# Optimization experiments

Hardware: AMD Instinct MI355X
Metric: run time of the kernel (lower is better)

Reference implementation:

```python
import jax, jax.numpy as jnp
import numpy as np

NUM = 8          # group_heads
ALPHA = 1000.0   # Pos_Enc alpha
BETA = 100.0     # Pos_Enc beta


def setup_inputs() -> dict:
    key = jax.random.key(0)
    ks = jax.random.split(key, 19)
    N, C, H = 16384, 64, 1024
    gs1 = H // NUM
    s = 0.02
    r = lambda k, shp: jax.random.normal(k, shp, dtype=jnp.float32) * s
    return {
        "features": jax.random.normal(ks[0], (N, C), dtype=jnp.float32),
        "fc1_w": r(ks[1], (C, H)), "fc1_b": r(ks[2], (H,)),
        "fc2_w": r(ks[3], (H, C)), "fc2_b": r(ks[4], (C,)),
        "g1_w": r(ks[5], (H, H)), "g1_b": r(ks[6], (H,)),
        "g2_w": r(ks[7], (H, H)), "g2_b": r(ks[8], (H,)),
        "gg1_w": r(ks[9], (gs1, gs1)), "gg1_b": r(ks[10], (gs1,)),
        "gg2_w": r(ks[11], (gs1, gs1)), "gg2_b": r(ks[12], (gs1,)),
        "wq": r(ks[13], (H, H)), "wk": r(ks[14], (H, H)), "wv": r(ks[15], (H, H)),
        "wq2": r(ks[16], (gs1, gs1)), "wk2": r(ks[17], (gs1, gs1)),
        "lpe": jax.random.normal(ks[18], (1,), dtype=jnp.float32) * 0.1,
    }


def _mlp(x, w1, b1, w2, b2):
    return jax.nn.relu(x @ w1 + b1) @ w2 + b2


def reference(features, fc1_w, fc1_b, fc2_w, fc2_b, g1_w, g1_b, g2_w, g2_b,
              gg1_w, gg1_b, gg2_w, gg2_b, wq, wk, wv, wq2, wk2, lpe):
    N, C = features.shape
    H = fc1_w.shape[1]
    gs1 = H // NUM   # feature-group size
    gs2 = N // NUM   # token-group size

    x = features @ fc1_w + fc1_b                      # (N, H)

    # --- attn1: per-feature-group vector attention (shared weights -> vectorized)
    xg = x.reshape(N, NUM, gs1)                       # contiguous feature slices
    q1 = xg @ wq2
    k1 = xg @ wk2
    h1 = _mlp(q1 - k1, gg1_w, gg1_b, gg2_w, gg2_b)
    attn1 = jax.nn.softmax(h1 / np.sqrt(gs1).astype(np.float32), axis=0)
    attn1 = attn1.reshape(N, H)                       # concat over groups = reshape

    # --- attn2: source bug: loop uses stale i=NUM-1, so the LAST token group
    # is processed NUM times and tiled along tokens.
    gf2 = x[(NUM - 1) * gs2:, :]                      # (gs2, H)
    q2 = gf2 @ wq
    k2 = gf2 @ wk
    h2 = _mlp(q2 - k2, g1_w, g1_b, g2_w, g2_b)
    a2 = jax.nn.softmax(h2 / np.sqrt(H).astype(np.float32), axis=0)
    attn2 = jnp.tile(a2, (NUM, 1))                    # (N, H)

    attn = attn1 + attn2
    v = x @ wv                                        # (N, H)

    # --- sinusoidal positional encoding (Pos_Enc), only coord-0 slice survives
    xyz = features[:, :3]                             # (N, 3)
    feat_dim = H // 2
    feat_range = jnp.arange(feat_dim, dtype=jnp.float32)
    dim_embed = jnp.power(jnp.float32(ALPHA), feat_range / feat_dim)
    div = BETA * xyz[..., None] / dim_embed           # (N, 3, feat_dim)
    emb = jnp.concatenate([jnp.sin(div), jnp.cos(div)], axis=-1)  # (N, 3, H)
    pe = (emb + lpe[0]) * lpe[0]
    pe0 = pe[:, 0, :]                                 # (N, H) first coordinate

    res = attn * (v + pe0)                            # elementwise einsum bmf,bmf->bmf
    out = res @ fc2_w + fc2_b + features              # residual
    return out
```

## Files before the change

kernel.cpp:

```cpp
#include <hip/hip_runtime.h>
#include <hip/hip_bf16.h>
#include <math.h>
#include <type_traits>


typedef __attribute__((ext_vector_type(8))) short short8;
typedef __attribute__((ext_vector_type(4))) float f32x4;
typedef __attribute__((ext_vector_type(4))) float float4v;

#define GLOAD_LDS16(gptr, lptr)                                                 \
    __builtin_amdgcn_global_load_lds(                                           \
        (const __attribute__((address_space(1))) void*)(gptr),                  \
        (__attribute__((address_space(3))) void*)(lptr), 16, 0, 0)

static __device__ __forceinline__ unsigned short f2bf_bits(float v) {
    __hip_bfloat16 h = __float2bfloat16(v);
    return __builtin_bit_cast(unsigned short, h);
}
static __device__ __forceinline__ float bf_bits2f(unsigned short u) {
    return __bfloat162float(__builtin_bit_cast(__hip_bfloat16, u));
}
static __device__ __forceinline__ int swz16(int r, int c16) {
    return (r << 4) + (c16 ^ (r & 7));
}
static __device__ __forceinline__ int swz_elem(int r, int c) {
    return (r << 7) + ((((c << 1) ^ ((r & 7) << 4))) >> 1);
}
static __device__ __forceinline__ int xcd_swz(int bid, int nwg) {
    return (bid & 7) * (nwg >> 3) + (bid >> 3);
}

static __device__ void conv_t_dev(const float* __restrict__ A, const float* __restrict__ Bsub,
                                  __hip_bfloat16* __restrict__ Ot, int K, int N,
                                  int bx, int by, int tid, float* t )
{
    const int n0 = bx * 32, k0 = by * 32;
    const int tx = tid & 31, ty = tid >> 5;
    #pragma unroll
    for (int j = 0; j < 4; ++j) {
        int k = k0 + ty + j * 8;
        float v = A[(long)k * N + n0 + tx];
        if (Bsub) v -= Bsub[(long)k * N + n0 + tx];
        t[(ty + j * 8) * 33 + tx] = v;
    }
    __syncthreads();
    #pragma unroll
    for (int j = 0; j < 4; ++j) {
        int n = n0 + ty + j * 8;
        Ot[(long)n * K + k0 + tx] = __float2bfloat16(t[tx * 33 + ty + j * 8]);
    }
}

static __device__ void xgemm_dev(const float* __restrict__ features,
                                 const float* __restrict__ fc1_w,
                                 const float* __restrict__ fc1_b,
                                 __hip_bfloat16* __restrict__ xb,
                                 int tile, int tid, char* smem)
{
    unsigned short* As = (unsigned short*)smem;
    unsigned short* Bs = (unsigned short*)(smem + 16384);
    const int bm = (tile >> 3) << 7, bn = (tile & 7) << 7;
    const int wid = tid >> 6, lane = tid & 63;
    const int wm = (wid >> 1) << 6, wn = (wid & 1) << 6;
    const int l15 = lane & 15, kg = lane >> 4;

    #pragma unroll
    for (int i = 0; i < 8; ++i) {
        int idx = i * 256 + tid;
        int r = idx >> 4, c4 = idx & 15;
        float4v f = *(const float4v*)(features + (long)(bm + r) * 64 + c4 * 4);
        unsigned int p0 = f2bf_bits(f[0]) | ((unsigned int)f2bf_bits(f[1]) << 16);
        unsigned int p1 = f2bf_bits(f[2]) | ((unsigned int)f2bf_bits(f[3]) << 16);
        int dst = r * 64 + (((c4 >> 1) ^ (r & 7)) << 3) + (c4 & 1) * 4;
        unsigned int* p = (unsigned int*)&As[dst];
        p[0] = p0; p[1] = p1;
    }
    #pragma unroll
    for (int i = 0; i < 8; ++i) {
        int idx = i * 256 + tid;
        int k = idx >> 5, c4b = idx & 31;
        float4v g = *(const float4v*)(fc1_w + (long)k * 1024 + bn + c4b * 4);
        #pragma unroll
        for (int q = 0; q < 4; ++q) {
            int n = c4b * 4 + q;
            Bs[n * 64 + (((k >> 3) ^ (n & 7)) << 3) + (k & 7)] = f2bf_bits(g[q]);
        }
    }
    __syncthreads();

    f32x4 acc[4][4] = {};
    #pragma unroll
    for (int ks2 = 0; ks2 < 2; ++ks2) {
        const int kslot = ks2 * 4 + kg;
        short8 af[4], bf_[4];
        #pragma unroll
        for (int m = 0; m < 4; ++m) {
            int r = wm + m * 16 + l15;
            af[m] = *(const short8*)&As[r * 64 + ((kslot ^ (r & 7)) << 3)];
        }
        #pragma unroll
        for (int n = 0; n < 4; ++n) {
            int r = wn + n * 16 + l15;
            bf_[n] = *(const short8*)&Bs[r * 64 + ((kslot ^ (r & 7)) << 3)];
        }
        #pragma unroll
        for (int m = 0; m < 4; ++m)
            #pragma unroll
            for (int n = 0; n < 4; ++n)
                acc[m][n] = __builtin_amdgcn_mfma_f32_16x16x32_bf16(
                    af[m], bf_[n], acc[m][n], 0, 0, 0);
    }
    const int rq = kg << 2;
    #pragma unroll
    for (int n = 0; n < 4; ++n) {
        const int col = bn + wn + n * 16 + l15;
        const float bv = fc1_b[col];
        #pragma unroll
        for (int m = 0; m < 4; ++m)
            #pragma unroll
            for (int j = 0; j < 4; ++j)
                xb[(long)(bm + wm + m * 16 + rq + j) * 1024 + col] =
                    __float2bfloat16(acc[m][n][j] + bv);
    }
}

__global__ __launch_bounds__(256) void prep_x_k(
    const float* __restrict__ features, const float* __restrict__ fc1_w,
    const float* __restrict__ fc1_b, const float* __restrict__ fc2_w,
    const float* __restrict__ fc2_b, const float* __restrict__ g1_w,
    const float* __restrict__ g2_w, const float* __restrict__ wq,
    const float* __restrict__ wk, const float* __restrict__ wv,
    const float* __restrict__ wq2, const float* __restrict__ wk2,
    const float* __restrict__ gg1_w, const float* __restrict__ gg2_w,
    __hip_bfloat16* __restrict__ fc2T, __hip_bfloat16* __restrict__ wdT,
    __hip_bfloat16* __restrict__ wvT, __hip_bfloat16* __restrict__ g1T,
    __hip_bfloat16* __restrict__ g2T, __hip_bfloat16* __restrict__ wd2T,
    __hip_bfloat16* __restrict__ gg1T, __hip_bfloat16* __restrict__ gg2T,
    __hip_bfloat16* __restrict__ xb, float* __restrict__ invde,
    float* __restrict__ out)
{
    __shared__ __align__(16) char smem[32768];
    float* t = (float*)smem;
    const int bid = blockIdx.x;
    const int tid = threadIdx.x;

    if (bid == 0) {
        #pragma unroll
        for (int i = 0; i < 2; ++i) {
            int idx = tid + i * 256;
            invde[idx] = exp2f(-9.96578428466209f * (float)idx * (1.f / 512.f));
        }
    } else if (bid < 257) {
        const float4v* f4 = (const float4v*)features;
        float4v* o4 = (float4v*)out;
        const float4v* b4 = (const float4v*)fc2_b;
        long base = (long)(bid - 1) * 1024;
        #pragma unroll
        for (int i = 0; i < 4; ++i) {
            long idx = base + tid + i * 256;
            o4[idx] = f4[idx] + b4[idx & 15];
        }
    } else if (bid < 1281) {
        int tt = bid - 257;  conv_t_dev(wq, wk, wdT, 1024, 1024, tt & 31, tt >> 5, tid, t);
    } else if (bid < 2305) {
        int tt = bid - 1281; conv_t_dev(wv, nullptr, wvT, 1024, 1024, tt & 31, tt >> 5, tid, t);
    } else if (bid < 3329) {
        int tt = bid - 2305; conv_t_dev(g1_w, nullptr, g1T, 1024, 1024, tt & 31, tt >> 5, tid, t);
    } else if (bid < 4353) {
        int tt = bid - 3329; conv_t_dev(g2_w, nullptr, g2T, 1024, 1024, tt & 31, tt >> 5, tid, t);
    } else if (bid < 4417) {
        int tt = bid - 4353; conv_t_dev(fc2_w, nullptr, fc2T, 1024, 64, tt & 1, tt >> 1, tid, t);
    } else if (bid < 4433) {
        int tt = bid - 4417; conv_t_dev(wq2, wk2, wd2T, 128, 128, tt & 3, tt >> 2, tid, t);
    } else if (bid < 4449) {
        int tt = bid - 4433; conv_t_dev(gg1_w, nullptr, gg1T, 128, 128, tt & 3, tt >> 2, tid, t);
    } else if (bid < 4465) {
        int tt = bid - 4449; conv_t_dev(gg2_w, nullptr, gg2T, 128, 128, tt & 3, tt >> 2, tid, t);
    } else {
        xgemm_dev(features, fc1_w, fc1_b, xb, bid - 4465, tid, smem);
    }
}

template <int OP, bool CS>
static __device__ void gemm6464_dev(
    const __hip_bfloat16* __restrict__ A, const __hip_bfloat16* __restrict__ Bt,
    const float* __restrict__ bias, __hip_bfloat16* __restrict__ Co,
    float scale, float* __restrict__ pcs, int swz, int tid, char* smem)
{
    const int wid = tid >> 6, lane = tid & 63;
    const int bm = (swz >> 4) << 6, bn = (swz & 15) << 6;
    const int wm = (wid >> 1) << 5, wn = (wid & 1) << 5;
    f32x4 acc[2][2] = {};
    const int l15 = lane & 15, kg = lane >> 4;
    const int rS = tid >> 2;
    const int c4s = (tid & 3) ^ ((rS >> 1) & 3);

#define G66_STAGE(b, k0)                                                        \
    { char* base = smem + (b) * 8192;                                           \
      GLOAD_LDS16(A + (long)(bm + rS) * 1024 + (k0) + c4s * 8,                  \
                  base + (wid << 6) * 16);                                      \
      GLOAD_LDS16(Bt + (long)(bn + rS) * 1024 + (k0) + c4s * 8,                 \
                  base + 4096 + (wid << 6) * 16); }

    G66_STAGE(0, 0);
    #pragma unroll 2
    for (int kt = 0; kt < 32; ++kt) {
        if (kt < 31) {
            G66_STAGE((kt + 1) & 1, (kt + 1) * 32);
            asm volatile("s_waitcnt vmcnt(2)" ::: "memory");
        } else {
            asm volatile("s_waitcnt vmcnt(0)" ::: "memory");
        }
        __builtin_amdgcn_s_barrier();
        __builtin_amdgcn_sched_barrier(0);
        const char* AsB = smem + (kt & 1) * 8192;
        const char* BsB = AsB + 4096;
        short8 af[2], bf_[2];
        #pragma unroll
        for (int m = 0; m < 2; ++m) {
            const int R = wm + m * 16 + l15;
            af[m] = *(const short8*)(AsB + R * 64 + ((kg ^ ((R >> 1) & 3)) << 4));
        }
        #pragma unroll
        for (int n = 0; n < 2; ++n) {
            const int R = wn + n * 16 + l15;
            bf_[n] = *(const short8*)(BsB + R * 64 + ((kg ^ ((R >> 1) & 3)) << 4));
        }
        __builtin_amdgcn_s_setprio(1);
        #pragma unroll
        for (int m = 0; m < 2; ++m)
            #pragma unroll
            for (int n = 0; n < 2; ++n)
                acc[m][n] = __builtin_amdgcn_mfma_f32_16x16x32_bf16(
                    af[m], bf_[n], acc[m][n], 0, 0, 0);
        __builtin_amdgcn_s_setprio(0);
        __builtin_amdgcn_s_barrier();
    }
#undef G66_STAGE

    const int rq = kg << 2;
    float csum[2];
    #pragma unroll
    for (int n = 0; n < 2; ++n) {
        const int col = bn + wn + n * 16 + l15;
        const float bv = bias ? bias[col] : 0.f;
        csum[n] = 0.f;
        #pragma unroll
        for (int m = 0; m < 2; ++m) {
            #pragma unroll
            for (int j = 0; j < 4; ++j) {
                const int row = bm + wm + m * 16 + rq + j;
                float cv = acc[m][n][j] + bv;
                if (OP == 1) cv = fmaxf(cv, 0.f);
                if (OP == 2) cv = __expf(cv * scale);
                if (CS) csum[n] += cv;
                Co[(long)row * 1024 + col] = __float2bfloat16(cv);
            }
        }
    }
    if (CS) {
        __syncthreads();
        float* ps = (float*)smem;
        const int slot = ((wid >> 1) << 2) | kg;
        #pragma unroll
        for (int n = 0; n < 2; ++n)
            ps[(wn + n * 16 + l15) * 8 + slot] = csum[n];
        __syncthreads();
        if (tid < 64) {
            float s = 0.f;
            #pragma unroll
            for (int q = 0; q < 8; ++q) s += ps[tid * 8 + q];
            pcs[(long)(swz >> 4) * 1024 + bn + tid] = s;
        }
    }
}

template <int OP, bool CS>
__global__ __launch_bounds__(256) void gemm6464_k(
    const __hip_bfloat16* __restrict__ A, const __hip_bfloat16* __restrict__ Bt,
    const float* __restrict__ bias, __hip_bfloat16* __restrict__ Co,
    float scale, float* __restrict__ pcs)
{
    __shared__ __align__(16) char smem[16384];
    const int swz = xcd_swz(blockIdx.y * gridDim.x + blockIdx.x, gridDim.x * gridDim.y);
    gemm6464_dev<OP, CS>(A, Bt, bias, Co, scale, pcs, swz, threadIdx.x, smem);
}

static __device__ void chain_dev(
    const __hip_bfloat16* __restrict__ xb,
    const __hip_bfloat16* __restrict__ w1T,
    const __hip_bfloat16* __restrict__ w2T,
    const __hip_bfloat16* __restrict__ w3T,
    const float* __restrict__ b2, const float* __restrict__ b3,
    __hip_bfloat16* __restrict__ e1, float* __restrict__ pcs1,
    int tileIdx, int tid, char* smem)
{
    unsigned short* act = (unsigned short*)smem;
    unsigned short* Wb  = (unsigned short*)(smem + 32768);
    const int wid = tid >> 6, lane = tid & 63;
    const int wm = (wid >> 1) << 6, wn = (wid & 1) << 6;
    const long tile = (long)tileIdx * (128 * 128);

    #pragma unroll
    for (int i = 0; i < 8; ++i) {
        int L = i * 256 + wid * 64 + lane;
        int r = L >> 4, c16o = (L & 15) ^ (r & 7);
        GLOAD_LDS16(xb + tile + r * 128 + c16o * 8,
                    (char*)act + (i * 256 + wid * 64) * 16);
        GLOAD_LDS16(w1T + r * 128 + c16o * 8,
                    (char*)Wb + (i * 256 + wid * 64) * 16);
    }
    __syncthreads();

    f32x4 acc[4][4];
    const int rq = (lane >> 4) << 2;

#define CHAIN_ZERO()                                                            \
    _Pragma("unroll") for (int m = 0; m < 4; ++m)                               \
        _Pragma("unroll") for (int n = 0; n < 4; ++n)                           \
            acc[m][n] = (f32x4){0.f, 0.f, 0.f, 0.f};

#define CHAIN_MM()                                                              \
    _Pragma("unroll") for (int ks = 0; ks < 4; ++ks) {                          \
        short8 af[4], bfv[4];                                                   \
        const int kc = ks * 4 + (lane >> 4);                                    \
        _Pragma("unroll") for (int m = 0; m < 4; ++m) {                         \
            int r = wm + m * 16 + (lane & 15);                                  \
            af[m] = *(const short8*)((const char*)act + swz16(r, kc) * 16);     \
        }                                                                       \
        _Pragma("unroll") for (int n = 0; n < 4; ++n) {                         \
            int r = wn + n * 16 + (lane & 15);                                  \
            bfv[n] = *(const short8*)((const char*)Wb + swz16(r, kc) * 16);     \
        }                                                                       \
        _Pragma("unroll") for (int m = 0; m < 4; ++m)                           \
            _Pragma("unroll") for (int n = 0; n < 4; ++n)                       \
                acc[m][n] = __builtin_amdgcn_mfma_f32_16x16x32_bf16(            \
                    af[m], bfv[n], acc[m][n], 0, 0, 0);                         \
    }

#define STAGE_W(wptr)                                                           \
    _Pragma("unroll") for (int i = 0; i < 8; ++i) {                             \
        int L = i * 256 + wid * 64 + lane;                                      \
        int r = L >> 4, c16o = (L & 15) ^ (r & 7);                              \
        GLOAD_LDS16((wptr) + r * 128 + c16o * 8,                                \
                    (char*)Wb + (i * 256 + wid * 64) * 16);                     \
    }

    CHAIN_ZERO(); CHAIN_MM();
    __syncthreads();
    STAGE_W(w2T);
    #pragma unroll
    for (int m = 0; m < 4; ++m)
        #pragma unroll
        for (int n = 0; n < 4; ++n)
            #pragma unroll
            for (int j = 0; j < 4; ++j) {
                int row = wm + m * 16 + rq + j, col = wn + n * 16 + (lane & 15);
                act[swz_elem(row, col)] = f2bf_bits(acc[m][n][j]);
            }
    __syncthreads();

    CHAIN_ZERO(); CHAIN_MM();
    __syncthreads();
    STAGE_W(w3T);
    {
        float bv[4];
        #pragma unroll
        for (int n = 0; n < 4; ++n) bv[n] = b2[wn + n * 16 + (lane & 15)];
        #pragma unroll
        for (int m = 0; m < 4; ++m)
            #pragma unroll
            for (int n = 0; n < 4; ++n)
                #pragma unroll
                for (int j = 0; j < 4; ++j) {
                    int row = wm + m * 16 + rq + j, col = wn + n * 16 + (lane & 15);
                    act[swz_elem(row, col)] = f2bf_bits(fmaxf(acc[m][n][j] + bv[n], 0.f));
                }
    }
    __syncthreads();

    CHAIN_ZERO(); CHAIN_MM();
    __syncthreads();
    {
        float bv[4];
        #pragma unroll
        for (int n = 0; n < 4; ++n) bv[n] = b3[wn + n * 16 + (lane & 15)];
        #pragma unroll
        for (int m = 0; m < 4; ++m)
            #pragma unroll
            for (int n = 0; n < 4; ++n)
                #pragma unroll
                for (int j = 0; j < 4; ++j) {
                    int row = wm + m * 16 + rq + j, col = wn + n * 16 + (lane & 15);
                    float ev = __expf((acc[m][n][j] + bv[n]) * 0.08838834764831845f);
                    act[swz_elem(row, col)] = f2bf_bits(ev);
                }
    }
    __syncthreads();

    #pragma unroll
    for (int i = 0; i < 8; ++i) {
        int idx = i * 256 + tid;
        int r = idx >> 4, c16o = idx & 15;
        short8 vd = *(const short8*)((const char*)act + swz16(r, c16o) * 16);
        *(short8*)((__hip_bfloat16*)e1 + tile + r * 128 + c16o * 8) = vd;
    }
    #pragma unroll
    for (int i = 0; i < 4; ++i) {
        int p = i * 256 + tid;
        int g = p >> 7, c = p & 127;
        float s = 0.f;
        #pragma unroll
        for (int t16 = 0; t16 < 16; ++t16) {
            int r = t16 * 8 + g;
            s += bf_bits2f(act[swz_elem(r, c)]);
        }
        pcs1[(long)tileIdx * 1024 + p] = s;
    }
#undef CHAIN_ZERO
#undef CHAIN_MM
#undef STAGE_W
}

__global__ __launch_bounds__(256) void mid_k(
    const __hip_bfloat16* __restrict__ xb, const __hip_bfloat16* __restrict__ wdT,
    __hip_bfloat16* __restrict__ d2b,
    const __hip_bfloat16* __restrict__ wd2T, const __hip_bfloat16* __restrict__ gg1T,
    const __hip_bfloat16* __restrict__ gg2T, const float* __restrict__ gg1_b,
    const float* __restrict__ gg2_b, __hip_bfloat16* __restrict__ e1,
    float* __restrict__ pcs1)
{
    __shared__ __align__(16) char smem[65536];
    const int bid = blockIdx.x, tid = threadIdx.x;
    if (bid < 512) {
        gemm6464_dev<0, false>(xb + (size_t)14336 * 1024, wdT, nullptr, d2b,
                               0.f, nullptr, xcd_swz(bid, 512), tid, smem);
    } else {
        chain_dev(xb, wd2T, gg1T, gg2T, gg1_b, gg2_b, e1, pcs1, bid - 512, tid, smem);
    }
}

__global__ __launch_bounds__(1024) void reduce_k(
    const float* __restrict__ pcs1, const float* __restrict__ pcs2,
    float* __restrict__ rcs1, float* __restrict__ rcs2)
{
    __shared__ float red[16][64];
    const int tx = threadIdx.x, ty = threadIdx.y;
    if (blockIdx.x < 16) {
        const int col = blockIdx.x * 64 + tx;
        float s = 0.f;
        for (int p = ty; p < 1024; p += 16) s += pcs1[(long)p * 1024 + col];
        red[ty][tx] = s;
        __syncthreads();
        if (ty == 0) {
            float t = 0.f;
            #pragma unroll
            for (int q = 0; q < 16; ++q) t += red[q][tx];
            rcs1[col] = 1.f / t;
        }
    } else {
        const int col = (blockIdx.x - 16) * 64 + tx;
        float s = 0.f;
        for (int p = ty; p < 32; p += 16) s += pcs2[(long)p * 1024 + col];
        red[ty][tx] = s;
        __syncthreads();
        if (ty == 0) {
            float t = 0.f;
            #pragma unroll
            for (int q = 0; q < 16; ++q) t += red[q][tx];
            rcs2[col] = 1.f / t;
        }
    }
}

__global__ __launch_bounds__(256) void gemm_v_res_out(
    const __hip_bfloat16* __restrict__ A, const __hip_bfloat16* __restrict__ Bt,
    const __hip_bfloat16* __restrict__ e1, const __hip_bfloat16* __restrict__ e2,
    const float* __restrict__ rcs1, const float* __restrict__ rcs2,
    const float* __restrict__ invde, const float* __restrict__ feats,
    const float* __restrict__ lpe, const __hip_bfloat16* __restrict__ fc2T,
    float* __restrict__ out)
{
    __shared__ __align__(16) char smem[34816];
    unsigned short* st = (unsigned short*)smem;

    const int tid = threadIdx.x;
    const int wid = tid >> 6;
    const int lane = tid & 63;
    const int swz = xcd_swz(blockIdx.y * gridDim.x + blockIdx.x, gridDim.x * gridDim.y);
    const int bm = (swz >> 3) << 7, bn = (swz & 7) << 7;
    const int wm = (wid >> 1) << 6, wn = (wid & 1) << 6;

    f32x4 acc[4][4] = {};
    const int l15 = lane & 15;
    const int kg = lane >> 4;
    const int arow = wm + l15;
    const int brow = wn + l15;

#define VR_STAGE(b, k0)                                                         \
    { char* base = smem + (b) * 16384;                                          \
      _Pragma("unroll") for (int i = 0; i < 2; ++i) {                           \
        const int idx = i * 256 + tid;                                          \
        const int r = idx >> 2;                                                 \
        const int c4s = (idx & 3) ^ ((r >> 1) & 3);                             \
        GLOAD_LDS16(A + (long)(bm + r) * 1024 + (k0) + c4s * 8,                 \
                    base + (i * 256 + wid * 64) * 16);                          \
        GLOAD_LDS16(Bt + (long)(bn + r) * 1024 + (k0) + c4s * 8,                \
                    base + 8192 + (i * 256 + wid * 64) * 16); } }

    VR_STAGE(0, 0);
    #pragma unroll 2
    for (int kt = 0; kt < 32; ++kt) {
        if (kt < 31) {
            VR_STAGE((kt + 1) & 1, (kt + 1) * 32);
            asm volatile("s_waitcnt vmcnt(4)" ::: "memory");
        } else {
            asm volatile("s_waitcnt vmcnt(0)" ::: "memory");
        }
        __builtin_amdgcn_s_barrier();
        __builtin_amdgcn_sched_barrier(0);
        const char* AsB = smem + (kt & 1) * 16384;
        const char* BsB = AsB + 8192;
        short8 af[4], bf_[4];
        #pragma unroll
        for (int m = 0; m < 4; ++m) {
            const int R = arow + m * 16;
            af[m] = *(const short8*)(AsB + R * 64 + ((kg ^ ((R >> 1) & 3)) << 4));
        }
        #pragma unroll
        for (int n = 0; n < 4; ++n) {
            const int R = brow + n * 16;
            bf_[n] = *(const short8*)(BsB + R * 64 + ((kg ^ ((R >> 1) & 3)) << 4));
        }
        __builtin_amdgcn_s_setprio(1);
        #pragma unroll
        for (int m = 0; m < 4; ++m)
            #pragma unroll
            for (int n = 0; n < 4; ++n)
                acc[m][n] = __builtin_amdgcn_mfma_f32_16x16x32_bf16(
                    af[m], bf_[n], acc[m][n], 0, 0, 0);
        __builtin_amdgcn_s_setprio(0);
        __builtin_amdgcn_s_barrier();
    }
#undef VR_STAGE

    const int rq = kg << 2;
    #pragma unroll
    for (int m = 0; m < 4; ++m)
        #pragma unroll
        for (int n = 0; n < 4; ++n)
            #pragma unroll
            for (int j = 0; j < 4; ++j)
                st[(wm + m * 16 + rq + j) * 136 + wn + n * 16 + l15] =
                    f2bf_bits(acc[m][n][j]);
    __syncthreads();

    const float lp = lpe[0];
    #pragma unroll
    for (int p = 0; p < 4; ++p) {
        const int r = p * 32 + (tid >> 3);
        const int cc = (tid & 7) << 4;
        const int grow = bm + r;
        const float angs = 100.f * feats[(long)grow * 64];
        const long goff = (long)grow * 1024 + bn + cc;
        const long goff2 = (long)(grow & 2047) * 1024 + bn + cc;
        short8 ev1[2], ev2[2], sv[2];
        ev1[0] = *(const short8*)((const unsigned short*)e1 + goff);
        ev1[1] = *(const short8*)((const unsigned short*)e1 + goff + 8);
        ev2[0] = *(const short8*)((const unsigned short*)e2 + goff2);
        ev2[1] = *(const short8*)((const unsigned short*)e2 + goff2 + 8);
        sv[0] = *(const short8*)&st[r * 136 + cc];
        sv[1] = *(const short8*)&st[r * 136 + cc + 8];
        unsigned short ov[16];
        #pragma unroll
        for (int q = 0; q < 16; ++q) {
            const int h = bn + cc + q;
            const float ang = angs * invde[h & 511];
            const float tr = (h < 512) ? __sinf(ang) : __cosf(ang);
            const float a = bf_bits2f((unsigned short)ev1[q >> 3][q & 7]) * rcs1[h] +
                            bf_bits2f((unsigned short)ev2[q >> 3][q & 7]) * rcs2[h];
            const float vv = bf_bits2f((unsigned short)sv[q >> 3][q & 7]);
            ov[q] = f2bf_bits(a * (vv + (tr + lp) * lp));
        }
        *(short8*)&st[r * 136 + cc] = *(short8*)&ov[0];
        *(short8*)&st[r * 136 + cc + 8] = *(short8*)&ov[8];
    }
    __syncthreads();

    {
        const int wmO = wid << 5;
        f32x4 aco[2][4] = {};
        #pragma unroll
        for (int ks = 0; ks < 4; ++ks) {
            short8 afo[2], bfo[4];
            #pragma unroll
            for (int m = 0; m < 2; ++m)
                afo[m] = *(const short8*)&st[(wmO + m * 16 + l15) * 136 + ks * 32 + kg * 8];
            #pragma unroll
            for (int n = 0; n < 4; ++n)
                bfo[n] = *(const short8*)((const unsigned short*)fc2T +
                                          (long)(n * 16 + l15) * 1024 + bn + ks * 32 + kg * 8);
            #pragma unroll
            for (int m = 0; m < 2; ++m)
                #pragma unroll
                for (int n = 0; n < 4; ++n)
                    aco[m][n] = __builtin_amdgcn_mfma_f32_16x16x32_bf16(
                        afo[m], bfo[n], aco[m][n], 0, 0, 0);
        }
        #pragma unroll
        for (int m = 0; m < 2; ++m)
            #pragma unroll
            for (int n = 0; n < 4; ++n)
                #pragma unroll
                for (int j = 0; j < 4; ++j) {
                    const int row = bm + wmO + m * 16 + rq + j;
                    atomicAdd(&out[(long)row * 64 + n * 16 + l15], aco[m][n][j]);
                }
    }
}

extern "C" void kernel_launch(void* const* d_in, const int* in_sizes, int n_in,
                              void* d_out, int out_size, void* d_ws, size_t ws_size,
                              hipStream_t stream) {
    const float* features = (const float*)d_in[0];
    const float* fc1_w = (const float*)d_in[1];
    const float* fc1_b = (const float*)d_in[2];
    const float* fc2_w = (const float*)d_in[3];
    const float* fc2_b = (const float*)d_in[4];
    const float* g1_w = (const float*)d_in[5];
    const float* g1_b = (const float*)d_in[6];
    const float* g2_w = (const float*)d_in[7];
    const float* g2_b = (const float*)d_in[8];
    const float* gg1_w = (const float*)d_in[9];
    const float* gg1_b = (const float*)d_in[10];
    const float* gg2_w = (const float*)d_in[11];
    const float* gg2_b = (const float*)d_in[12];
    const float* wq = (const float*)d_in[13];
    const float* wk = (const float*)d_in[14];
    const float* wv = (const float*)d_in[15];
    const float* wq2 = (const float*)d_in[16];
    const float* wk2 = (const float*)d_in[17];
    const float* lpe = (const float*)d_in[18];
    float* out = (float*)d_out;

    char* ws = (char*)d_ws;
    const size_t MB = 1024ull * 1024ull;
    __hip_bfloat16* xb   = (__hip_bfloat16*)ws;
    __hip_bfloat16* e1   = (__hip_bfloat16*)(ws + 32 * MB);
    __hip_bfloat16* d2b  = (__hip_bfloat16*)(ws + 64 * MB);
    __hip_bfloat16* t2b  = (__hip_bfloat16*)(ws + 68 * MB);
    __hip_bfloat16* e2b  = (__hip_bfloat16*)(ws + 72 * MB);
    float*          pcs1 = (float*)(ws + 76 * MB);
    float*          pcs2 = (float*)(ws + 80 * MB);
    char* W = ws + 81 * MB;
    __hip_bfloat16* wdT   = (__hip_bfloat16*)W;
    __hip_bfloat16* wvT   = (__hip_bfloat16*)(W + 2 * MB);
    __hip_bfloat16* g1T   = (__hip_bfloat16*)(W + 4 * MB);
    __hip_bfloat16* g2T   = (__hip_bfloat16*)(W + 6 * MB);
    __hip_bfloat16* fc2T  = (__hip_bfloat16*)(W + 8 * MB);
    __hip_bfloat16* wd2T  = (__hip_bfloat16*)(W + 8 * MB + 256 * 1024);
    __hip_bfloat16* gg1T  = (__hip_bfloat16*)(W + 8 * MB + 320 * 1024);
    __hip_bfloat16* gg2T  = (__hip_bfloat16*)(W + 8 * MB + 384 * 1024);
    float* rcs1  = (float*)(W + 9 * MB);
    float* rcs2  = rcs1 + 1024;
    float* invde = rcs2 + 1024;

    prep_x_k<<<5489, 256, 0, stream>>>(
        features, fc1_w, fc1_b, fc2_w, fc2_b, g1_w, g2_w, wq, wk, wv, wq2, wk2,
        gg1_w, gg2_w, fc2T, wdT, wvT, g1T, g2T, wd2T, gg1T, gg2T, xb, invde, out);

    mid_k<<<1536, 256, 0, stream>>>(xb, wdT, d2b, wd2T, gg1T, gg2T,
                                    gg1_b, gg2_b, e1, pcs1);

    gemm6464_k<1, false><<<dim3(16, 32), 256, 0, stream>>>(d2b, g1T, g1_b, t2b, 0.f, nullptr);
    gemm6464_k<2, true><<<dim3(16, 32), 256, 0, stream>>>(t2b, g2T, g2_b, e2b, 0.03125f, pcs2);

    reduce_k<<<32, dim3(64, 16), 0, stream>>>(pcs1, pcs2, rcs1, rcs2);

    gemm_v_res_out<<<dim3(8, 128), 256, 0, stream>>>(
        xb, wvT, e1, e2b, rcs1, rcs2, invde, features, lpe, fc2T, out);
}
```

Measured before the change: 300.7 us.

## Split fused prep/mid kernels into separate launches and deepen vres K-tile

Splits the combined prep+xgemm kernel into a weight-transpose kernel, where each block now handles four 32x32 sub-tiles, and a separate fc1 GEMM kernel. The mixed mid kernel is split into its t1 GEMM and chain kernels, and the GEMM template launches are replaced by dedicated wrappers. The final V/residual GEMM moves from 32-wide to 64-wide K stages with 64KB of LDS and an 8-way swizzle, halving loop iterations and barriers. This trades fewer syncs and more uniform blocks for extra launches and higher LDS use, which may reduce occupancy.

```diff
diff --git a/kernel.cpp b/kernel.cpp
--- a/kernel.cpp
+++ b/kernel.cpp
@@ -34,31 +34,89 @@
                                   __hip_bfloat16* __restrict__ Ot, int K, int N,
                                   int bx, int by, int tid, float* t )
 {
-    const int n0 = bx * 32, k0 = by * 32;
+    const int n0 = bx * 32, k0 = by * 128;
     const int tx = tid & 31, ty = tid >> 5;
-    #pragma unroll
-    for (int j = 0; j < 4; ++j) {
-        int k = k0 + ty + j * 8;
-        float v = A[(long)k * N + n0 + tx];
-        if (Bsub) v -= Bsub[(long)k * N + n0 + tx];
-        t[(ty + j * 8) * 33 + tx] = v;
-    }
-    __syncthreads();
-    #pragma unroll
-    for (int j = 0; j < 4; ++j) {
-        int n = n0 + ty + j * 8;
-        Ot[(long)n * K + k0 + tx] = __float2bfloat16(t[tx * 33 + ty + j * 8]);
-    }
-}
-
-static __device__ void xgemm_dev(const float* __restrict__ features,
-                                 const float* __restrict__ fc1_w,
-                                 const float* __restrict__ fc1_b,
-                                 __hip_bfloat16* __restrict__ xb,
-                                 int tile, int tid, char* smem)
-{
+    const int ksub = (K - k0 < 128) ? (K - k0) / 32 : 4;
+    for (int s = 0; s < ksub; ++s) {
+        const int kk = k0 + s * 32;
+        #pragma unroll
+        for (int j = 0; j < 4; ++j) {
+            int k = kk + ty + j * 8;
+            float v = A[(long)k * N + n0 + tx];
+            if (Bsub) v -= Bsub[(long)k * N + n0 + tx];
+            t[(ty + j * 8) * 33 + tx] = v;
+        }
+        __syncthreads();
+        #pragma unroll
+        for (int j = 0; j < 4; ++j) {
+            int n = n0 + ty + j * 8;
+            Ot[(long)n * K + kk + tx] = __float2bfloat16(t[tx * 33 + ty + j * 8]);
+        }
+        __syncthreads();
+    }
+}
+
+__global__ __launch_bounds__(256) void prep_k(
+    const float* __restrict__ features, const float* __restrict__ fc2_w,
+    const float* __restrict__ fc2_b, const float* __restrict__ g1_w,
+    const float* __restrict__ g2_w, const float* __restrict__ wq,
+    const float* __restrict__ wk, const float* __restrict__ wv,
+    const float* __restrict__ wq2, const float* __restrict__ wk2,
+    const float* __restrict__ gg1_w, const float* __restrict__ gg2_w,
+    __hip_bfloat16* __restrict__ fc2T, __hip_bfloat16* __restrict__ wdT,
+    __hip_bfloat16* __restrict__ wvT, __hip_bfloat16* __restrict__ g1T,
+    __hip_bfloat16* __restrict__ g2T, __hip_bfloat16* __restrict__ wd2T,
+    __hip_bfloat16* __restrict__ gg1T, __hip_bfloat16* __restrict__ gg2T,
+    float* __restrict__ invde, float* __restrict__ out)
+{
+    __shared__ float t[32 * 33];
+    const int bid = blockIdx.x;
+    const int tid = threadIdx.x;
+
+    if (bid == 0) {
+        #pragma unroll
+        for (int i = 0; i < 2; ++i) {
+            int idx = tid + i * 256;
+            invde[idx] = exp2f(-9.96578428466209f * (float)idx * (1.f / 512.f));
+        }
+    } else if (bid < 257) {
+        const float4v* f4 = (const float4v*)features;
+        float4v* o4 = (float4v*)out;
+        const float4v* b4 = (const float4v*)fc2_b;
+        long base = (long)(bid - 1) * 1024;
+        #pragma unroll
+        for (int i = 0; i < 4; ++i) {
+            long idx = base + tid + i * 256;
+            o4[idx] = f4[idx] + b4[idx & 15];
+        }
+    } else if (bid < 513) {
+        int tt = bid - 257;  conv_t_dev(wq, wk, wdT, 1024, 1024, tt & 31, tt >> 5, tid, t);
+    } else if (bid < 769) {
+        int tt = bid - 513;  conv_t_dev(wv, nullptr, wvT, 1024, 1024, tt & 31, tt >> 5, tid, t);
+    } else if (bid < 1025) {
+        int tt = bid - 769;  conv_t_dev(g1_w, nullptr, g1T, 1024, 1024, tt & 31, tt >> 5, tid, t);
+    } else if (bid < 1281) {
+        int tt = bid - 1025; conv_t_dev(g2_w, nullptr, g2T, 1024, 1024, tt & 31, tt >> 5, tid, t);
+    } else if (bid < 1297) {
+        int tt = bid - 1281; conv_t_dev(fc2_w, nullptr, fc2T, 1024, 64, tt & 1, tt >> 1, tid, t);
+    } else if (bid < 1301) {
+        int tt = bid - 1297; conv_t_dev(wq2, wk2, wd2T, 128, 128, tt & 3, 0, tid, t);
+    } else if (bid < 1305) {
+        int tt = bid - 1301; conv_t_dev(gg1_w, nullptr, gg1T, 128, 128, tt & 3, 0, tid, t);
+    } else {
+        int tt = bid - 1305; conv_t_dev(gg2_w, nullptr, gg2T, 128, 128, tt & 3, 0, tid, t);
+    }
+}
+
+__global__ __launch_bounds__(256) void xgemm_k(
+    const float* __restrict__ features, const float* __restrict__ fc1_w,
+    const float* __restrict__ fc1_b, __hip_bfloat16* __restrict__ xb)
+{
+    __shared__ __align__(16) char smem[32768];
     unsigned short* As = (unsigned short*)smem;
     unsigned short* Bs = (unsigned short*)(smem + 16384);
+    const int tile = blockIdx.x;
+    const int tid = threadIdx.x;
     const int bm = (tile >> 3) << 7, bn = (tile & 7) << 7;
     const int wid = tid >> 6, lane = tid & 63;
     const int wm = (wid >> 1) << 6, wn = (wid & 1) << 6;
@@ -124,63 +182,6 @@
     }
 }
 
-__global__ __launch_bounds__(256) void prep_x_k(
-    const float* __restrict__ features, const float* __restrict__ fc1_w,
-    const float* __restrict__ fc1_b, const float* __restrict__ fc2_w,
-    const float* __restrict__ fc2_b, const float* __restrict__ g1_w,
-    const float* __restrict__ g2_w, const float* __restrict__ wq,
-    const float* __restrict__ wk, const float* __restrict__ wv,
-    const float* __restrict__ wq2, const float* __restrict__ wk2,
-    const float* __restrict__ gg1_w, const float* __restrict__ gg2_w,
-    __hip_bfloat16* __restrict__ fc2T, __hip_bfloat16* __restrict__ wdT,
-    __hip_bfloat16* __restrict__ wvT, __hip_bfloat16* __restrict__ g1T,
-    __hip_bfloat16* __restrict__ g2T, __hip_bfloat16* __restrict__ wd2T,
-    __hip_bfloat16* __restrict__ gg1T, __hip_bfloat16* __restrict__ gg2T,
-    __hip_bfloat16* __restrict__ xb, float* __restrict__ invde,
-    float* __restrict__ out)
-{
-    __shared__ __align__(16) char smem[32768];
-    float* t = (float*)smem;
-    const int bid = blockIdx.x;
-    const int tid = threadIdx.x;
-
-    if (bid == 0) {
-        #pragma unroll
-        for (int i = 0; i < 2; ++i) {
-            int idx = tid + i * 256;
-            invde[idx] = exp2f(-9.96578428466209f * (float)idx * (1.f / 512.f));
-        }
-    } else if (bid < 257) {
-        const float4v* f4 = (const float4v*)features;
-        float4v* o4 = (float4v*)out;
-        const float4v* b4 = (const float4v*)fc2_b;
-        long base = (long)(bid - 1) * 1024;
-        #pragma unroll
-        for (int i = 0; i < 4; ++i) {
-            long idx = base + tid + i * 256;
-            o4[idx] = f4[idx] + b4[idx & 15];
-        }
-    } else if (bid < 1281) {
-        int tt = bid - 257;  conv_t_dev(wq, wk, wdT, 1024, 1024, tt & 31, tt >> 5, tid, t);
-    } else if (bid < 2305) {
-        int tt = bid - 1281; conv_t_dev(wv, nullptr, wvT, 1024, 1024, tt & 31, tt >> 5, tid, t);
-    } else if (bid < 3329) {
-        int tt = bid - 2305; conv_t_dev(g1_w, nullptr, g1T, 1024, 1024, tt & 31, tt >> 5, tid, t);
-    } else if (bid < 4353) {
-        int tt = bid - 3329; conv_t_dev(g2_w, nullptr, g2T, 1024, 1024, tt & 31, tt >> 5, tid, t);
-    } else if (bid < 4417) {
-        int tt = bid - 4353; conv_t_dev(fc2_w, nullptr, fc2T, 1024, 64, tt & 1, tt >> 1, tid, t);
-    } else if (bid < 4433) {
-        int tt = bid - 4417; conv_t_dev(wq2, wk2, wd2T, 128, 128, tt & 3, tt >> 2, tid, t);
-    } else if (bid < 4449) {
-        int tt = bid - 4433; conv_t_dev(gg1_w, nullptr, gg1T, 128, 128, tt & 3, tt >> 2, tid, t);
-    } else if (bid < 4465) {
-        int tt = bid - 4449; conv_t_dev(gg2_w, nullptr, gg2T, 128, 128, tt & 3, tt >> 2, tid, t);
-    } else {
-        xgemm_dev(features, fc1_w, fc1_b, xb, bid - 4465, tid, smem);
-    }
-}
-
 template <int OP, bool CS>
 static __device__ void gemm6464_dev(
     const __hip_bfloat16* __restrict__ A, const __hip_bfloat16* __restrict__ Bt,
@@ -275,30 +276,47 @@
     }
 }
 
-template <int OP, bool CS>
-__global__ __launch_bounds__(256) void gemm6464_k(
+__global__ __launch_bounds__(256) void t1_k(
+    const __hip_bfloat16* __restrict__ A, const __hip_bfloat16* __restrict__ Bt,
+    __hip_bfloat16* __restrict__ Co)
+{
+    __shared__ __align__(16) char smem[16384];
+    const int swz = xcd_swz(blockIdx.y * gridDim.x + blockIdx.x, gridDim.x * gridDim.y);
+    gemm6464_dev<0, false>(A, Bt, nullptr, Co, 0.f, nullptr, swz, threadIdx.x, smem);
+}
+__global__ __launch_bounds__(256) void t2_k(
+    const __hip_bfloat16* __restrict__ A, const __hip_bfloat16* __restrict__ Bt,
+    const float* __restrict__ bias, __hip_bfloat16* __restrict__ Co)
+{
+    __shared__ __align__(16) char smem[16384];
+    const int swz = xcd_swz(blockIdx.y * gridDim.x + blockIdx.x, gridDim.x * gridDim.y);
+    gemm6464_dev<1, false>(A, Bt, bias, Co, 0.f, nullptr, swz, threadIdx.x, smem);
+}
+__global__ __launch_bounds__(256) void t3_k(
     const __hip_bfloat16* __restrict__ A, const __hip_bfloat16* __restrict__ Bt,
     const float* __restrict__ bias, __hip_bfloat16* __restrict__ Co,
-    float scale, float* __restrict__ pcs)
+    float* __restrict__ pcs)
 {
     __shared__ __align__(16) char smem[16384];
     const int swz = xcd_swz(blockIdx.y * gridDim.x + blockIdx.x, gridDim.x * gridDim.y);
-    gemm6464_dev<OP, CS>(A, Bt, bias, Co, scale, pcs, swz, threadIdx.x, smem);
-}
-
-static __device__ void chain_dev(
+    gemm6464_dev<2, true>(A, Bt, bias, Co, 0.03125f, pcs, swz, threadIdx.x, smem);
+}
+
+__global__ __launch_bounds__(256) void chain_k(
     const __hip_bfloat16* __restrict__ xb,
     const __hip_bfloat16* __restrict__ w1T,
     const __hip_bfloat16* __restrict__ w2T,
     const __hip_bfloat16* __restrict__ w3T,
     const float* __restrict__ b2, const float* __restrict__ b3,
-    __hip_bfloat16* __restrict__ e1, float* __restrict__ pcs1,
-    int tileIdx, int tid, char* smem)
-{
+    __hip_bfloat16* __restrict__ e1, float* __restrict__ pcs1)
+{
+    __shared__ __align__(16) char smem[65536];
     unsigned short* act = (unsigned short*)smem;
     unsigned short* Wb  = (unsigned short*)(smem + 32768);
+    const int tid = threadIdx.x;
     const int wid = tid >> 6, lane = tid & 63;
     const int wm = (wid >> 1) << 6, wn = (wid & 1) << 6;
+    const int tileIdx = blockIdx.x;
     const long tile = (long)tileIdx * (128 * 128);
 
     #pragma unroll
@@ -422,24 +440,6 @@
 #undef STAGE_W
 }
 
-__global__ __launch_bounds__(256) void mid_k(
-    const __hip_bfloat16* __restrict__ xb, const __hip_bfloat16* __restrict__ wdT,
-    __hip_bfloat16* __restrict__ d2b,
-    const __hip_bfloat16* __restrict__ wd2T, const __hip_bfloat16* __restrict__ gg1T,
-    const __hip_bfloat16* __restrict__ gg2T, const float* __restrict__ gg1_b,
-    const float* __restrict__ gg2_b, __hip_bfloat16* __restrict__ e1,
-    float* __restrict__ pcs1)
-{
-    __shared__ __align__(16) char smem[65536];
-    const int bid = blockIdx.x, tid = threadIdx.x;
-    if (bid < 512) {
-        gemm6464_dev<0, false>(xb + (size_t)14336 * 1024, wdT, nullptr, d2b,
-                               0.f, nullptr, xcd_swz(bid, 512), tid, smem);
-    } else {
-        chain_dev(xb, wd2T, gg1T, gg2T, gg1_b, gg2_b, e1, pcs1, bid - 512, tid, smem);
-    }
-}
-
 __global__ __launch_bounds__(1024) void reduce_k(
     const float* __restrict__ pcs1, const float* __restrict__ pcs2,
     float* __restrict__ rcs1, float* __restrict__ rcs2)
@@ -473,7 +473,7 @@
     }
 }
 
-__global__ __launch_bounds__(256) void gemm_v_res_out(
+__global__ __launch_bounds__(256) void vres_k(
     const __hip_bfloat16* __restrict__ A, const __hip_bfloat16* __restrict__ Bt,
     const __hip_bfloat16* __restrict__ e1, const __hip_bfloat16* __restrict__ e2,
     const float* __restrict__ rcs1, const float* __restrict__ rcs2,
@@ -481,7 +481,7 @@
     const float* __restrict__ lpe, const __hip_bfloat16* __restrict__ fc2T,
     float* __restrict__ out)
 {
-    __shared__ __align__(16) char smem[34816];
+    __shared__ __align__(16) char smem[65536];
     unsigned short* st = (unsigned short*)smem;
 
     const int tid = threadIdx.x;
@@ -492,53 +492,57 @@
     const int wm = (wid >> 1) << 6, wn = (wid & 1) << 6;
 
     f32x4 acc[4][4] = {};
+    const int c8 = tid & 7;
     const int l15 = lane & 15;
     const int kg = lane >> 4;
     const int arow = wm + l15;
     const int brow = wn + l15;
 
 #define VR_STAGE(b, k0)                                                         \
-    { char* base = smem + (b) * 16384;                                          \
-      _Pragma("unroll") for (int i = 0; i < 2; ++i) {                           \
-        const int idx = i * 256 + tid;                                          \
-        const int r = idx >> 2;                                                 \
-        const int c4s = (idx & 3) ^ ((r >> 1) & 3);                             \
-        GLOAD_LDS16(A + (long)(bm + r) * 1024 + (k0) + c4s * 8,                 \
+    { char* base = smem + (b) * 32768;                                          \
+      _Pragma("unroll") for (int i = 0; i < 4; ++i) {                           \
+        const int r = i * 32 + (tid >> 3);                                      \
+        const int c8s = c8 ^ (r & 7);                                           \
+        GLOAD_LDS16(A + (long)(bm + r) * 1024 + (k0) + c8s * 8,                 \
                     base + (i * 256 + wid * 64) * 16);                          \
-        GLOAD_LDS16(Bt + (long)(bn + r) * 1024 + (k0) + c4s * 8,                \
-                    base + 8192 + (i * 256 + wid * 64) * 16); } }
+        GLOAD_LDS16(Bt + (long)(bn + r) * 1024 + (k0) + c8s * 8,                \
+                    base + 16384 + (i * 256 + wid * 64) * 16); } }
 
     VR_STAGE(0, 0);
     #pragma unroll 2
-    for (int kt = 0; kt < 32; ++kt) {
-        if (kt < 31) {
-            VR_STAGE((kt + 1) & 1, (kt + 1) * 32);
-            asm volatile("s_waitcnt vmcnt(4)" ::: "memory");
+    for (int kt = 0; kt < 16; ++kt) {
+        if (kt < 15) {
+            VR_STAGE((kt + 1) & 1, (kt + 1) * 64);
+            asm volatile("s_waitcnt vmcnt(8)" ::: "memory");
         } else {
             asm volatile("s_waitcnt vmcnt(0)" ::: "memory");
         }
         __builtin_amdgcn_s_barrier();
         __builtin_amdgcn_sched_barrier(0);
-        const char* AsB = smem + (kt & 1) * 16384;
-        const char* BsB = AsB + 8192;
-        short8 af[4], bf_[4];
-        #pragma unroll
-        for (int m = 0; m < 4; ++m) {
-            const int R = arow + m * 16;
-            af[m] = *(const short8*)(AsB + R * 64 + ((kg ^ ((R >> 1) & 3)) << 4));
-        }
-        #pragma unroll
-        for (int n = 0; n < 4; ++n) {
-            const int R = brow + n * 16;
-            bf_[n] = *(const short8*)(BsB + R * 64 + ((kg ^ ((R >> 1) & 3)) << 4));
-        }
+        const __hip_bfloat16* As = (const __hip_bfloat16*)(smem + (kt & 1) * 32768);
+        const __hip_bfloat16* Bs = (const __hip_bfloat16*)(smem + (kt & 1) * 32768 + 16384);
         __builtin_amdgcn_s_setprio(1);
         #pragma unroll
-        for (int m = 0; m < 4; ++m)
-            #pragma unroll
-            for (int n = 0; n < 4; ++n)
-                acc[m][n] = __builtin_amdgcn_mfma_f32_16x16x32_bf16(
-                    af[m], bf_[n], acc[m][n], 0, 0, 0);
+        for (int ks2 = 0; ks2 < 2; ++ks2) {
+            const int kslot = ks2 * 4 + kg;
+            short8 af[4], bf_[4];
+            #pragma unroll
+            for (int m = 0; m < 4; ++m) {
+                const int r = arow + m * 16;
+                af[m] = *(const short8*)(As + (r * 8 + (kslot ^ (r & 7))) * 8);
+            }
+            #pragma unroll
+            for (int n = 0; n < 4; ++n) {
+                const int r = brow + n * 16;
+                bf_[n] = *(const short8*)(Bs + (r * 8 + (kslot ^ (r & 7))) * 8);
+            }
+            #pragma unroll
+            for (int m = 0; m < 4; ++m)
+                #pragma unroll
+                for (int n = 0; n < 4; ++n)
+                    acc[m][n] = __builtin_amdgcn_mfma_f32_16x16x32_bf16(
+                        af[m], bf_[n], acc[m][n], 0, 0, 0);
+        }
         __builtin_amdgcn_s_setprio(0);
         __builtin_amdgcn_s_barrier();
     }
@@ -665,18 +669,21 @@
     float* rcs2  = rcs1 + 1024;
     float* invde = rcs2 + 1024;
 
-    prep_x_k<<<5489, 256, 0, stream>>>(
-        features, fc1_w, fc1_b, fc2_w, fc2_b, g1_w, g2_w, wq, wk, wv, wq2, wk2,
-        gg1_w, gg2_w, fc2T, wdT, wvT, g1T, g2T, wd2T, gg1T, gg2T, xb, invde, out);
-
-    mid_k<<<1536, 256, 0, stream>>>(xb, wdT, d2b, wd2T, gg1T, gg2T,
-                                    gg1_b, gg2_b, e1, pcs1);
-
-    gemm6464_k<1, false><<<dim3(16, 32), 256, 0, stream>>>(d2b, g1T, g1_b, t2b, 0.f, nullptr);
-    gemm6464_k<2, true><<<dim3(16, 32), 256, 0, stream>>>(t2b, g2T, g2_b, e2b, 0.03125f, pcs2);
+    prep_k<<<1309, 256, 0, stream>>>(
+        features, fc2_w, fc2_b, g1_w, g2_w, wq, wk, wv, wq2, wk2,
+        gg1_w, gg2_w, fc2T, wdT, wvT, g1T, g2T, wd2T, gg1T, gg2T, invde, out);
+
+    xgemm_k<<<1024, 256, 0, stream>>>(features, fc1_w, fc1_b, xb);
+
+    t1_k<<<dim3(16, 32), 256, 0, stream>>>(xb + (size_t)14336 * 1024, wdT, d2b);
+
+    chain_k<<<1024, 256, 0, stream>>>(xb, wd2T, gg1T, gg2T, gg1_b, gg2_b, e1, pcs1);
+
+    t2_k<<<dim3(16, 32), 256, 0, stream>>>(d2b, g1T, g1_b, t2b);
+    t3_k<<<dim3(16, 32), 256, 0, stream>>>(t2b, g2T, g2_b, e2b, pcs2);
 
     reduce_k<<<32, dim3(64, 16), 0, stream>>>(pcs1, pcs2, rcs1, rcs2);
 
-    gemm_v_res_out<<<dim3(8, 128), 256, 0, stream>>>(
+    vres_k<<<dim3(8, 128), 256, 0, stream>>>(
         xb, wvT, e1, e2b, rcs1, rcs2, invde, features, lpe, fc2T, out);
 }
```

New measurement: 289.9 us. 3.6% less time.
